# Kernel tuning notes

Hardware: AMD Instinct MI355X
Metric: run time of the kernel (lower is better)

## Reference

```python
import jax, jax.numpy as jnp
import numpy as np

WINDOW = 128
LOOK_BACKWARD = 1
LOOK_FORWARD = 0
PAD_VALUE = -1


def look_around(x, backward=LOOK_BACKWARD, forward=LOOK_FORWARD, pad_value=PAD_VALUE):
    # x: [b, windows, window_size, ...]; pad along windows axis, concat along window_size axis
    pad_width = [(0, 0)] * x.ndim
    pad_width[1] = (backward, forward)
    px = jnp.pad(x, pad_width, constant_values=pad_value)
    w = x.shape[1]
    return jnp.concatenate([px[:, i:i + w] for i in range(forward + backward + 1)], axis=2)


def rotate_half(x):
    x1, x2 = jnp.split(x, 2, axis=-1)
    return jnp.concatenate([-x2, x1], axis=-1)


def setup_inputs() -> dict:
    key = jax.random.key(0)
    k1, k2, k3 = jax.random.split(key, 3)
    B, H, N, D = 4, 16, 4096, 64
    return {
        "q": jax.random.normal(k1, (B, H, N, D), dtype=jnp.float32),
        "k": jax.random.normal(k2, (B, H, N, D), dtype=jnp.float32),
        "v": jax.random.normal(k3, (B, H, N, D), dtype=jnp.float32),
    }


def reference(q, k, v):
    B, H, N, D = q.shape
    qf = q.reshape(B * H, N, D)
    kf = k.reshape(B * H, N, D)
    vf = v.reshape(B * H, N, D)

    # --- inline rotary (SinusoidalEmbeddings + apply_rotary_pos_emb) ---
    inv_freq = 1.0 / (10000.0 ** (jnp.arange(0, D, 2, dtype=jnp.float32) / D))  # [D/2]
    t = jnp.arange(N, dtype=jnp.float32)
    half = t[:, None] * inv_freq[None, :]                      # [N, D/2]
    freqs = jnp.concatenate([half, half], axis=-1)             # [N, D]
    cos, sin = jnp.cos(freqs), jnp.sin(freqs)
    qf = qf * cos + rotate_half(qf) * sin
    kf = kf * cos + rotate_half(kf) * sin

    # --- blocked local attention ---
    w = WINDOW
    windows = N // w
    scale = D ** -0.5
    bq = qf.reshape(B * H, windows, w, D)
    bk = look_around(kf.reshape(B * H, windows, w, D))         # [bh, windows, j, D]
    bv = look_around(vf.reshape(B * H, windows, w, D))

    seq = jnp.arange(N).reshape(1, windows, w)
    bq_t = seq[..., :, None]                                   # [1, windows, w, 1]
    bq_k = look_around(seq)[..., None, :]                      # [1, windows, 1, j]

    sim = jnp.einsum('bwie,bwje->bwij', bq, bk) * scale        # [bh, windows, w, j]
    mask_value = -jnp.finfo(sim.dtype).max
    sim = jnp.where(bq_t < bq_k, mask_value, sim)              # causal mask

    attn = jax.nn.softmax(sim, axis=-1)
    out = jnp.einsum('bwij,bwje->bwie', attn, bv)              # [bh, windows, w, D]
    return out.reshape(B, H, N, D)
```

## Files before the change

kernel.cpp:

```cpp
#include <hip/hip_runtime.h>
#include <hip/hip_bf16.h>

typedef __attribute__((ext_vector_type(8))) short    short8;
typedef __attribute__((ext_vector_type(4))) short    short4v;
typedef __attribute__((ext_vector_type(4))) float    float4v;
typedef __attribute__((ext_vector_type(2))) unsigned uint2v;
typedef __attribute__((ext_vector_type(4))) unsigned uint4v;

#define MFMA_QK(A,B,C) __builtin_amdgcn_mfma_f32_16x16x32_bf16(A,B,C,0,0,0)
#define MFMA_PV(A,B,C) __builtin_amdgcn_mfma_f32_16x16x16bf16_1k(A,B,C,0,0,0)

#define N_ 4096
#define D_ 64
#define W_ 128
#define QSCALE 0.18033688011112042f

static __device__ __forceinline__ unsigned pk2(float a, float b) {
  unsigned ua = __float_as_uint(a) + 0x8000u;
  unsigned ub = __float_as_uint(b) + 0x8000u;
  return __builtin_amdgcn_perm(ub, ua, 0x07060302u);
}
static __device__ __forceinline__ void rope_sc(float rev, float& sn, float& cs) {
  float fr = __builtin_amdgcn_fractf(rev);
  sn = __builtin_amdgcn_sinf(fr);
  cs = __builtin_amdgcn_cosf(fr);
}
static __device__ __forceinline__ float invfreq_rev(int idx) {
  return __builtin_amdgcn_exp2f(-0.41524101186092034f * (float)idx) * 0.15915494309189535f;
}

__global__ __launch_bounds__(256, 3)
void la_fused(const float* __restrict__ qg, const float* __restrict__ kg,
              const float* __restrict__ vg, float* __restrict__ outg)
{
  __shared__ __attribute__((aligned(16))) short Kl[256][72];
  __shared__ __attribute__((aligned(16))) short Vt[32][68][4];

  const int blk  = blockIdx.x;
  const int w    = blk & 31;
  const int bh   = blk >> 5;
  const int base = bh * (N_ * D_);
  const int tid  = threadIdx.x;
  const int lane = tid & 63;
  const int wv   = tid >> 6;
  const int il   = lane & 15;
  const int qd   = lane >> 4;

  {
    const float* kb = kg + base;
    const int d0 = (tid & 7) << 2;
    float fr4[4];
#pragma unroll
    for (int dd = 0; dd < 4; ++dd) fr4[dd] = invfreq_rev(d0 + dd);
#pragma unroll
    for (int it = 0; it < 8; ++it) {
      int j = it * 32 + (tid >> 3);
      int g = w * W_ - W_ + j;
      uint2v w0, w1;
      if (g < 0) {
        w0 = uint2v{0xBF80BF80u, 0xBF80BF80u}; w1 = w0;
      } else {
        float4v a = *(const float4v*)(kb + g * D_ + d0);
        float4v b = *(const float4v*)(kb + g * D_ + d0 + 32);
        const float t = (float)g;
        float lo[4], hi[4];
#pragma unroll
        for (int dd = 0; dd < 4; ++dd) {
          float sn, cs; rope_sc(t * fr4[dd], sn, cs);
          lo[dd] = a[dd] * cs - b[dd] * sn;
          hi[dd] = b[dd] * cs + a[dd] * sn;
        }
        w0 = uint2v{ pk2(lo[0], lo[1]), pk2(lo[2], lo[3]) };
        w1 = uint2v{ pk2(hi[0], hi[1]), pk2(hi[2], hi[3]) };
      }
      *(uint2v*)&Kl[j][d0]      = w0;
      *(uint2v*)&Kl[j][d0 + 32] = w1;
    }
  }

  uint2v V2r[2][4];
  {
    const float* vb = vg + base;
    const int m  = tid & 15;
    const int d0 = m << 2;
#pragma unroll
    for (int pv = 0; pv < 4; ++pv) {
      int j0 = ((tid >> 4) + pv * 16) << 2;
      int g0 = w * W_ - W_ + j0;
      float vv[4][4];
      if (pv < 2 && g0 < 0) {
#pragma unroll
        for (int rr = 0; rr < 4; ++rr)
#pragma unroll
          for (int cc = 0; cc < 4; ++cc) vv[rr][cc] = -1.0f;
      } else {
#pragma unroll
        for (int rr = 0; rr < 4; ++rr) {
          float4v r = *(const float4v*)(vb + (g0 + rr) * D_ + d0);
          vv[rr][0]=r[0]; vv[rr][1]=r[1]; vv[rr][2]=r[2]; vv[rr][3]=r[3];
        }
      }
#pragma unroll
      for (int dd = 0; dd < 4; ++dd) {
        int cc = (dd + m) & 3;
        uint2v pw = uint2v{ pk2(vv[0][cc], vv[1][cc]), pk2(vv[2][cc], vv[3][cc]) };
        if (pv < 2) *(uint2v*)&Vt[j0 >> 2][d0 + cc][0] = pw;
        else        V2r[pv - 2][dd] = pw;
      }
    }
  }

  short8 qf[2][2];
  {
    float fr8[8];
#pragma unroll
    for (int jj = 0; jj < 8; ++jj) fr8[jj] = invfreq_rev(qd * 8 + jj);
#pragma unroll
    for (int ii = 0; ii < 2; ++ii) {
      const int n = w * W_ + wv * 32 + ii * 16 + il;
      const float* qr = qg + base + n * D_ + qd * 8;
      float4v x0 = *(const float4v*)(qr);
      float4v x1 = *(const float4v*)(qr + 4);
      float4v y0 = *(const float4v*)(qr + 32);
      float4v y1 = *(const float4v*)(qr + 36);
      const float t = (float)n;
      float lo[8], hi[8];
#pragma unroll
      for (int jj = 0; jj < 8; ++jj) {
        float xx = ((jj < 4) ? x0[jj & 3] : x1[jj & 3]) * QSCALE;
        float yy = ((jj < 4) ? y0[jj & 3] : y1[jj & 3]) * QSCALE;
        float sn, cs; rope_sc(t * fr8[jj], sn, cs);
        lo[jj] = xx * cs - yy * sn;
        hi[jj] = yy * cs + xx * sn;
      }
      uint4v pa = uint4v{ pk2(lo[0],lo[1]), pk2(lo[2],lo[3]), pk2(lo[4],lo[5]), pk2(lo[6],lo[7]) };
      uint4v pb = uint4v{ pk2(hi[0],hi[1]), pk2(hi[2],hi[3]), pk2(hi[4],hi[5]), pk2(hi[6],hi[7]) };
      qf[ii][0] = __builtin_bit_cast(short8, pa);
      qf[ii][1] = __builtin_bit_cast(short8, pb);
    }
  }

  __syncthreads();

  short4v P[2][16];
  float   invsum[2];
#pragma unroll
  for (int ii = 0; ii < 2; ++ii) {
    const int tmax = 8 + 2 * wv + ii;
    float4v S[16];
#pragma unroll
    for (int t = 0; t < 16; ++t) {
      if (t <= tmax) {
        short8 a0 = *(const short8*)&Kl[t * 16 + il][qd * 8];
        short8 a1 = *(const short8*)&Kl[t * 16 + il][32 + qd * 8];
        float4v z = {0.f, 0.f, 0.f, 0.f};
        z = MFMA_QK(a0, qf[ii][0], z);
        S[t] = MFMA_QK(a1, qf[ii][1], z);
      }
    }
    float sum = 0.0f;
#pragma unroll
    for (int t = 0; t < 16; ++t) {
      if (t <= tmax) {
        float p0 = __builtin_amdgcn_exp2f(S[t][0]);
        float p1 = __builtin_amdgcn_exp2f(S[t][1]);
        float p2 = __builtin_amdgcn_exp2f(S[t][2]);
        float p3 = __builtin_amdgcn_exp2f(S[t][3]);
        if (t == tmax) {
          if (qd * 4 + 0 > il) p0 = 0.f;
          if (qd * 4 + 1 > il) p1 = 0.f;
          if (qd * 4 + 2 > il) p2 = 0.f;
          if (qd * 4 + 3 > il) p3 = 0.f;
        }
        sum += (p0 + p1) + (p2 + p3);
        uint2v pw = uint2v{ pk2(p0, p1), pk2(p2, p3) };
        P[ii][t] = __builtin_bit_cast(short4v, pw);
      }
    }
    sum += __shfl_xor(sum, 16);
    sum += __shfl_xor(sum, 32);
    invsum[ii] = __builtin_amdgcn_rcpf(sum);
  }

  float4v O[2][4];
#pragma unroll
  for (int ii = 0; ii < 2; ++ii)
#pragma unroll
    for (int dt = 0; dt < 4; ++dt) { float4v z = {0.f,0.f,0.f,0.f}; O[ii][dt] = z; }

#pragma unroll
  for (int c = 0; c < 8; ++c) {
    short4v af[4];
#pragma unroll
    for (int dt = 0; dt < 4; ++dt)
      af[dt] = *(const short4v*)&Vt[c * 4 + qd][dt * 16 + il][0];
#pragma unroll
    for (int dt = 0; dt < 4; ++dt) {
      O[0][dt] = MFMA_PV(af[dt], P[0][c], O[0][dt]);
      O[1][dt] = MFMA_PV(af[dt], P[1][c], O[1][dt]);
    }
  }

  __syncthreads();
  {
    const int m  = tid & 15;
    const int d0 = m << 2;
#pragma unroll
    for (int pv = 0; pv < 2; ++pv) {
      int chunk = ((tid >> 4) + pv * 16);
#pragma unroll
      for (int dd = 0; dd < 4; ++dd) {
        int cc = (dd + m) & 3;
        *(uint2v*)&Vt[chunk][d0 + cc][0] = V2r[pv][dd];
      }
    }
  }
  __syncthreads();

  const int tmax0 = 8 + 2 * wv;
#pragma unroll
  for (int c = 8; c < 16; ++c) {
    if (c <= tmax0 + 1) {
      short4v af[4];
#pragma unroll
      for (int dt = 0; dt < 4; ++dt)
        af[dt] = *(const short4v*)&Vt[(c - 8) * 4 + qd][dt * 16 + il][0];
#pragma unroll
      for (int dt = 0; dt < 4; ++dt) {
        if (c <= tmax0) O[0][dt] = MFMA_PV(af[dt], P[0][c], O[0][dt]);
        O[1][dt] = MFMA_PV(af[dt], P[1][c], O[1][dt]);
      }
    }
  }

#pragma unroll
  for (int ii = 0; ii < 2; ++ii) {
    const int n = w * W_ + wv * 32 + ii * 16 + il;
    float* op = outg + base + n * D_;
    const float inv = invsum[ii];
#pragma unroll
    for (int dt = 0; dt < 4; ++dt) {
      float4v o = O[ii][dt];
      o[0] *= inv; o[1] *= inv; o[2] *= inv; o[3] *= inv;
      *(float4v*)(op + dt * 16 + qd * 4) = o;
    }
  }
}

extern "C" void kernel_launch(void* const* d_in, const int* in_sizes, int n_in,
                              void* d_out, int out_size, void* d_ws, size_t ws_size,
                              hipStream_t stream)
{
  const float* q = (const float*)d_in[0];
  const float* k = (const float*)d_in[1];
  const float* v = (const float*)d_in[2];
  float* out = (float*)d_out;
  la_fused<<<dim3(64 * 32), dim3(256), 0, stream>>>(q, k, v, out);
}
```

Baseline: 251.9 us.

## Process four consecutive windows per block, reusing K/V halves and prefetching next

Each block now handles four consecutive windows of one head, keeping a ring of two K/V segments in shared memory. Each K/V segment is loaded and rotary-encoded once and reused by the following window, instead of being rebuilt by a second block. Global loads for the next segment are issued into registers before the current window's attention, to hide latency. The price is fewer blocks (512 instead of 2048), lower occupancy bounds, more registers and extra barriers per window.

```diff
diff --git a/kernel.cpp b/kernel.cpp
--- a/kernel.cpp
+++ b/kernel.cpp
@@ -13,6 +13,7 @@
 #define N_ 4096
 #define D_ 64
 #define W_ 128
+#define WPB 4
 #define QSCALE 0.18033688011112042f
 
 static __device__ __forceinline__ unsigned pk2(float a, float b) {
@@ -29,16 +30,17 @@
   return __builtin_amdgcn_exp2f(-0.41524101186092034f * (float)idx) * 0.15915494309189535f;
 }
 
-__global__ __launch_bounds__(256, 3)
+__global__ __launch_bounds__(256, 2)
 void la_fused(const float* __restrict__ qg, const float* __restrict__ kg,
               const float* __restrict__ vg, float* __restrict__ outg)
 {
-  __shared__ __attribute__((aligned(16))) short Kl[256][72];
-  __shared__ __attribute__((aligned(16))) short Vt[32][68][4];
+  __shared__ __attribute__((aligned(16))) short Kseg[2][128][72];
+  __shared__ __attribute__((aligned(16))) short Vt[2][32][68][4];
 
   const int blk  = blockIdx.x;
-  const int w    = blk & 31;
-  const int bh   = blk >> 5;
+  const int wg   = blk & 7;
+  const int bh   = blk >> 3;
+  const int w0   = wg * WPB;
   const int base = bh * (N_ * D_);
   const int tid  = threadIdx.x;
   const int lane = tid & 63;
@@ -46,75 +48,76 @@
   const int il   = lane & 15;
   const int qd   = lane >> 4;
 
-  {
-    const float* kb = kg + base;
-    const int d0 = (tid & 7) << 2;
-    float fr4[4];
-#pragma unroll
-    for (int dd = 0; dd < 4; ++dd) fr4[dd] = invfreq_rev(d0 + dd);
-#pragma unroll
-    for (int it = 0; it < 8; ++it) {
-      int j = it * 32 + (tid >> 3);
-      int g = w * W_ - W_ + j;
-      uint2v w0, w1;
-      if (g < 0) {
-        w0 = uint2v{0xBF80BF80u, 0xBF80BF80u}; w1 = w0;
+  const float* kb = kg + base;
+  const float* vb = vg + base;
+
+  const int kd0 = (tid & 7) << 2;
+  const int kjw = tid >> 3;
+  const int vm  = tid & 15;
+  const int vd0 = vm << 2;
+  const int vjc = tid >> 4;
+  float kfr[4], qfr[8];
+#pragma unroll
+  for (int dd = 0; dd < 4; ++dd) kfr[dd] = invfreq_rev(kd0 + dd);
+#pragma unroll
+  for (int jj = 0; jj < 8; ++jj) qfr[jj] = invfreq_rev(qd * 8 + jj);
+
+  auto kRow = [&](int seg, int j, float4v a, float4v b, float t, bool pad) {
+    uint2v w0v, w1v;
+    if (pad) { w0v = uint2v{0xBF80BF80u, 0xBF80BF80u}; w1v = w0v; }
+    else {
+      float lo[4], hi[4];
+#pragma unroll
+      for (int dd = 0; dd < 4; ++dd) {
+        float sn, cs; rope_sc(t * kfr[dd], sn, cs);
+        lo[dd] = a[dd] * cs - b[dd] * sn;
+        hi[dd] = b[dd] * cs + a[dd] * sn;
+      }
+      w0v = uint2v{ pk2(lo[0], lo[1]), pk2(lo[2], lo[3]) };
+      w1v = uint2v{ pk2(hi[0], hi[1]), pk2(hi[2], hi[3]) };
+    }
+    *(uint2v*)&Kseg[seg][j][kd0]      = w0v;
+    *(uint2v*)&Kseg[seg][j][kd0 + 32] = w1v;
+  };
+  auto stageK = [&](int seg, int grow0) {
+#pragma unroll
+    for (int u = 0; u < 4; ++u) {
+      int j = u * 32 + kjw, g = grow0 + j;
+      float4v a = {0,0,0,0}, b = {0,0,0,0};
+      if (g >= 0) {
+        a = *(const float4v*)(kb + g * D_ + kd0);
+        b = *(const float4v*)(kb + g * D_ + kd0 + 32);
+      }
+      kRow(seg, j, a, b, (float)g, g < 0);
+    }
+  };
+  auto vChunk = [&](int seg, int ch, const float4v vv[4]) {
+#pragma unroll
+    for (int dd = 0; dd < 4; ++dd) {
+      int cc = (dd + vm) & 3;
+      uint2v pw = uint2v{ pk2(vv[0][cc], vv[1][cc]), pk2(vv[2][cc], vv[3][cc]) };
+      *(uint2v*)&Vt[seg][ch][vd0 + cc][0] = pw;
+    }
+  };
+  auto stageV = [&](int seg, int grow0) {
+#pragma unroll
+    for (int pvi = 0; pvi < 2; ++pvi) {
+      int ch = vjc + pvi * 16, g0 = grow0 + ch * 4;
+      float4v vv[4];
+      if (g0 < 0) {
+        float4v m1 = {-1.f,-1.f,-1.f,-1.f};
+#pragma unroll
+        for (int rr = 0; rr < 4; ++rr) vv[rr] = m1;
       } else {
-        float4v a = *(const float4v*)(kb + g * D_ + d0);
-        float4v b = *(const float4v*)(kb + g * D_ + d0 + 32);
-        const float t = (float)g;
-        float lo[4], hi[4];
-#pragma unroll
-        for (int dd = 0; dd < 4; ++dd) {
-          float sn, cs; rope_sc(t * fr4[dd], sn, cs);
-          lo[dd] = a[dd] * cs - b[dd] * sn;
-          hi[dd] = b[dd] * cs + a[dd] * sn;
-        }
-        w0 = uint2v{ pk2(lo[0], lo[1]), pk2(lo[2], lo[3]) };
-        w1 = uint2v{ pk2(hi[0], hi[1]), pk2(hi[2], hi[3]) };
-      }
-      *(uint2v*)&Kl[j][d0]      = w0;
-      *(uint2v*)&Kl[j][d0 + 32] = w1;
-    }
-  }
-
-  uint2v V2r[2][4];
-  {
-    const float* vb = vg + base;
-    const int m  = tid & 15;
-    const int d0 = m << 2;
-#pragma unroll
-    for (int pv = 0; pv < 4; ++pv) {
-      int j0 = ((tid >> 4) + pv * 16) << 2;
-      int g0 = w * W_ - W_ + j0;
-      float vv[4][4];
-      if (pv < 2 && g0 < 0) {
-#pragma unroll
-        for (int rr = 0; rr < 4; ++rr)
-#pragma unroll
-          for (int cc = 0; cc < 4; ++cc) vv[rr][cc] = -1.0f;
-      } else {
-#pragma unroll
-        for (int rr = 0; rr < 4; ++rr) {
-          float4v r = *(const float4v*)(vb + (g0 + rr) * D_ + d0);
-          vv[rr][0]=r[0]; vv[rr][1]=r[1]; vv[rr][2]=r[2]; vv[rr][3]=r[3];
-        }
-      }
-#pragma unroll
-      for (int dd = 0; dd < 4; ++dd) {
-        int cc = (dd + m) & 3;
-        uint2v pw = uint2v{ pk2(vv[0][cc], vv[1][cc]), pk2(vv[2][cc], vv[3][cc]) };
-        if (pv < 2) *(uint2v*)&Vt[j0 >> 2][d0 + cc][0] = pw;
-        else        V2r[pv - 2][dd] = pw;
-      }
-    }
-  }
+#pragma unroll
+        for (int rr = 0; rr < 4; ++rr) vv[rr] = *(const float4v*)(vb + (g0 + rr) * D_ + vd0);
+      }
+      vChunk(seg, ch, vv);
+    }
+  };
 
   short8 qf[2][2];
-  {
-    float fr8[8];
-#pragma unroll
-    for (int jj = 0; jj < 8; ++jj) fr8[jj] = invfreq_rev(qd * 8 + jj);
+  auto buildQ = [&](int w) {
 #pragma unroll
     for (int ii = 0; ii < 2; ++ii) {
       const int n = w * W_ + wv * 32 + ii * 16 + il;
@@ -129,7 +132,7 @@
       for (int jj = 0; jj < 8; ++jj) {
         float xx = ((jj < 4) ? x0[jj & 3] : x1[jj & 3]) * QSCALE;
         float yy = ((jj < 4) ? y0[jj & 3] : y1[jj & 3]) * QSCALE;
-        float sn, cs; rope_sc(t * fr8[jj], sn, cs);
+        float sn, cs; rope_sc(t * qfr[jj], sn, cs);
         lo[jj] = xx * cs - yy * sn;
         hi[jj] = yy * cs + xx * sn;
       }
@@ -138,111 +141,126 @@
       qf[ii][0] = __builtin_bit_cast(short8, pa);
       qf[ii][1] = __builtin_bit_cast(short8, pb);
     }
-  }
-
+  };
+
+  stageK(w0 & 1,       w0 * W_ - W_);
+  stageK((w0 + 1) & 1, w0 * W_);
+  stageV(w0 & 1,       w0 * W_ - W_);
+  stageV((w0 + 1) & 1, w0 * W_);
+  buildQ(w0);
   __syncthreads();
 
-  short4v P[2][16];
-  float   invsum[2];
-#pragma unroll
-  for (int ii = 0; ii < 2; ++ii) {
-    const int tmax = 8 + 2 * wv + ii;
-    float4v S[16];
-#pragma unroll
-    for (int t = 0; t < 16; ++t) {
-      if (t <= tmax) {
-        short8 a0 = *(const short8*)&Kl[t * 16 + il][qd * 8];
-        short8 a1 = *(const short8*)&Kl[t * 16 + il][32 + qd * 8];
-        float4v z = {0.f, 0.f, 0.f, 0.f};
-        z = MFMA_QK(a0, qf[ii][0], z);
-        S[t] = MFMA_QK(a1, qf[ii][1], z);
-      }
-    }
-    float sum = 0.0f;
-#pragma unroll
-    for (int t = 0; t < 16; ++t) {
-      if (t <= tmax) {
-        float p0 = __builtin_amdgcn_exp2f(S[t][0]);
-        float p1 = __builtin_amdgcn_exp2f(S[t][1]);
-        float p2 = __builtin_amdgcn_exp2f(S[t][2]);
-        float p3 = __builtin_amdgcn_exp2f(S[t][3]);
-        if (t == tmax) {
-          if (qd * 4 + 0 > il) p0 = 0.f;
-          if (qd * 4 + 1 > il) p1 = 0.f;
-          if (qd * 4 + 2 > il) p2 = 0.f;
-          if (qd * 4 + 3 > il) p3 = 0.f;
+  float4v pkr[8];
+  float4v pvr[8];
+
+#pragma unroll
+  for (int wi = 0; wi < WPB; ++wi) {
+    const int w  = w0 + wi;
+    const int sA = w & 1, sB = (w + 1) & 1;
+    const bool last = (wi == WPB - 1);
+
+    if (!last) {
+      const int grow0 = (w + 1) * W_;
+#pragma unroll
+      for (int u = 0; u < 4; ++u) {
+        int g = grow0 + u * 32 + kjw;
+        pkr[2*u]   = *(const float4v*)(kb + g * D_ + kd0);
+        pkr[2*u+1] = *(const float4v*)(kb + g * D_ + kd0 + 32);
+      }
+#pragma unroll
+      for (int pvi = 0; pvi < 2; ++pvi) {
+        int g0 = grow0 + (vjc + pvi * 16) * 4;
+#pragma unroll
+        for (int rr = 0; rr < 4; ++rr)
+          pvr[pvi*4+rr] = *(const float4v*)(vb + (g0 + rr) * D_ + vd0);
+      }
+    }
+
+    short4v P[2][16];
+    float   invsum[2];
+#pragma unroll
+    for (int ii = 0; ii < 2; ++ii) {
+      const int tmax = 8 + 2 * wv + ii;
+      float sum = 0.0f;
+#pragma unroll
+      for (int t = 0; t < 16; ++t) {
+        if (t <= tmax) {
+          const short* kr = (t < 8) ? &Kseg[sA][t * 16 + il][0]
+                                    : &Kseg[sB][(t - 8) * 16 + il][0];
+          short8 a0 = *(const short8*)(kr + qd * 8);
+          short8 a1 = *(const short8*)(kr + 32 + qd * 8);
+          float4v z = {0.f, 0.f, 0.f, 0.f};
+          z = MFMA_QK(a0, qf[ii][0], z);
+          z = MFMA_QK(a1, qf[ii][1], z);
+          float p0 = __builtin_amdgcn_exp2f(z[0]);
+          float p1 = __builtin_amdgcn_exp2f(z[1]);
+          float p2 = __builtin_amdgcn_exp2f(z[2]);
+          float p3 = __builtin_amdgcn_exp2f(z[3]);
+          if (t == tmax) {
+            if (qd * 4 + 0 > il) p0 = 0.f;
+            if (qd * 4 + 1 > il) p1 = 0.f;
+            if (qd * 4 + 2 > il) p2 = 0.f;
+            if (qd * 4 + 3 > il) p3 = 0.f;
+          }
+          sum += (p0 + p1) + (p2 + p3);
+          uint2v pw = uint2v{ pk2(p0, p1), pk2(p2, p3) };
+          P[ii][t] = __builtin_bit_cast(short4v, pw);
         }
-        sum += (p0 + p1) + (p2 + p3);
-        uint2v pw = uint2v{ pk2(p0, p1), pk2(p2, p3) };
-        P[ii][t] = __builtin_bit_cast(short4v, pw);
-      }
-    }
-    sum += __shfl_xor(sum, 16);
-    sum += __shfl_xor(sum, 32);
-    invsum[ii] = __builtin_amdgcn_rcpf(sum);
-  }
-
-  float4v O[2][4];
-#pragma unroll
-  for (int ii = 0; ii < 2; ++ii)
-#pragma unroll
-    for (int dt = 0; dt < 4; ++dt) { float4v z = {0.f,0.f,0.f,0.f}; O[ii][dt] = z; }
-
-#pragma unroll
-  for (int c = 0; c < 8; ++c) {
-    short4v af[4];
-#pragma unroll
-    for (int dt = 0; dt < 4; ++dt)
-      af[dt] = *(const short4v*)&Vt[c * 4 + qd][dt * 16 + il][0];
-#pragma unroll
-    for (int dt = 0; dt < 4; ++dt) {
-      O[0][dt] = MFMA_PV(af[dt], P[0][c], O[0][dt]);
-      O[1][dt] = MFMA_PV(af[dt], P[1][c], O[1][dt]);
-    }
-  }
-
-  __syncthreads();
-  {
-    const int m  = tid & 15;
-    const int d0 = m << 2;
-#pragma unroll
-    for (int pv = 0; pv < 2; ++pv) {
-      int chunk = ((tid >> 4) + pv * 16);
-#pragma unroll
-      for (int dd = 0; dd < 4; ++dd) {
-        int cc = (dd + m) & 3;
-        *(uint2v*)&Vt[chunk][d0 + cc][0] = V2r[pv][dd];
-      }
-    }
-  }
-  __syncthreads();
-
-  const int tmax0 = 8 + 2 * wv;
-#pragma unroll
-  for (int c = 8; c < 16; ++c) {
-    if (c <= tmax0 + 1) {
-      short4v af[4];
-#pragma unroll
-      for (int dt = 0; dt < 4; ++dt)
-        af[dt] = *(const short4v*)&Vt[(c - 8) * 4 + qd][dt * 16 + il][0];
+      }
+      sum += __shfl_xor(sum, 16);
+      sum += __shfl_xor(sum, 32);
+      invsum[ii] = __builtin_amdgcn_rcpf(sum);
+    }
+
+    float4v O[2][4];
+#pragma unroll
+    for (int ii = 0; ii < 2; ++ii)
+#pragma unroll
+      for (int dt = 0; dt < 4; ++dt) { float4v z = {0.f,0.f,0.f,0.f}; O[ii][dt] = z; }
+    const int cmax0 = 8 + 2 * wv;
+#pragma unroll
+    for (int c = 0; c < 16; ++c) {
+      if (c <= cmax0 + 1) {
+        short4v af[4];
+#pragma unroll
+        for (int dt = 0; dt < 4; ++dt)
+          af[dt] = *(const short4v*)&Vt[c < 8 ? sA : sB][(c & 7) * 4 + qd][dt * 16 + il][0];
+#pragma unroll
+        for (int dt = 0; dt < 4; ++dt) {
+          if (c <= cmax0) O[0][dt] = MFMA_PV(af[dt], P[0][c], O[0][dt]);
+          O[1][dt] = MFMA_PV(af[dt], P[1][c], O[1][dt]);
+        }
+      }
+    }
+
+#pragma unroll
+    for (int ii = 0; ii < 2; ++ii) {
+      const int n = w * W_ + wv * 32 + ii * 16 + il;
+      float* op = outg + base + n * D_;
+      const float inv = invsum[ii];
 #pragma unroll
       for (int dt = 0; dt < 4; ++dt) {
-        if (c <= tmax0) O[0][dt] = MFMA_PV(af[dt], P[0][c], O[0][dt]);
-        O[1][dt] = MFMA_PV(af[dt], P[1][c], O[1][dt]);
-      }
-    }
-  }
-
-#pragma unroll
-  for (int ii = 0; ii < 2; ++ii) {
-    const int n = w * W_ + wv * 32 + ii * 16 + il;
-    float* op = outg + base + n * D_;
-    const float inv = invsum[ii];
-#pragma unroll
-    for (int dt = 0; dt < 4; ++dt) {
-      float4v o = O[ii][dt];
-      o[0] *= inv; o[1] *= inv; o[2] *= inv; o[3] *= inv;
-      *(float4v*)(op + dt * 16 + qd * 4) = o;
+        float4v o = O[ii][dt];
+        o[0] *= inv; o[1] *= inv; o[2] *= inv; o[3] *= inv;
+        *(float4v*)(op + dt * 16 + qd * 4) = o;
+      }
+    }
+
+    if (!last) {
+      __syncthreads();
+      const int grow0 = (w + 1) * W_;
+#pragma unroll
+      for (int u = 0; u < 4; ++u)
+        kRow(sA, u * 32 + kjw, pkr[2*u], pkr[2*u+1], (float)(grow0 + u * 32 + kjw), false);
+#pragma unroll
+      for (int pvi = 0; pvi < 2; ++pvi) {
+        float4v vv[4];
+#pragma unroll
+        for (int rr = 0; rr < 4; ++rr) vv[rr] = pvr[pvi*4+rr];
+        vChunk(sA, vjc + pvi * 16, vv);
+      }
+      buildQ(w + 1);
+      __syncthreads();
     }
   }
 }
@@ -255,5 +273,5 @@
   const float* k = (const float*)d_in[1];
   const float* v = (const float*)d_in[2];
   float* out = (float*)d_out;
-  la_fused<<<dim3(64 * 32), dim3(256), 0, stream>>>(q, k, v, out);
-}
+  la_fused<<<dim3(64 * 8), dim3(256), 0, stream>>>(q, k, v, out);
+}
```

Result: faster. 230.0 us (-8.7%).
